# Optimization experiments

Measured on AMD Instinct MI355X. Metric: run time of the kernel, lower is better.

## Reference

```python
import jax, jax.numpy as jnp
import numpy as np

FACTORS = (16, 8, 8)          # prod == n_embd == 1024
H, DK = 16, 64
FACTOR_PARAMS = tuple(f * (f - 1) // 2 for f in FACTORS)  # (120, 28, 28)
DV = sum(FACTOR_PARAMS)       # 176
DVP = 256                     # next power of two padding
B, T, C = 2, 2048, 1024
OFFSET = 64


def _skew_exp(params, f):
    """params: (..., f*(f-1)//2) -> rotation matrices (..., f, f) via expm of skew-sym."""
    rows, cols = np.triu_indices(f, k=1)
    batch = params.shape[:-1]
    mat = jnp.zeros(batch + (f, f), jnp.float32).at[..., rows, cols].set(params.astype(jnp.float32))
    S = mat - jnp.swapaxes(mat, -1, -2)
    R = jax.vmap(jax.scipy.linalg.expm)(S.reshape((-1, f, f)))
    return R.reshape(batch + (f, f))


def setup_inputs() -> dict:
    key = jax.random.key(0)
    k1, k2, k3, k4, k5 = jax.random.split(key, 5)
    return {
        "x": jax.random.normal(k1, (B, T, C), jnp.float32),
        "cached_k": jax.random.normal(k2, (B, H, OFFSET, DK), jnp.float32),
        "cached_v": jax.random.normal(k3, (B, H, OFFSET, DVP), jnp.float32),
        "W_QK": jax.random.normal(k4, (2 * H * DK, C), jnp.float32) * 0.02,
        "W_V": jax.random.normal(k5, (H * DV, C), jnp.float32) * 0.02,
    }


def reference(x, cached_k, cached_v, W_QK, W_V):
    Bx, Tx, Cx = x.shape
    qk = x @ W_QK.T                                  # (B,T,2*H*DK)
    q, k = jnp.split(qk, 2, axis=-1)
    q = q.reshape(Bx, Tx, H, DK).transpose(0, 2, 1, 3)   # (B,H,T,DK)
    k = k.reshape(Bx, Tx, H, DK).transpose(0, 2, 1, 3)
    v = (x @ W_V.T).reshape(Bx, Tx, H, DV).transpose(0, 2, 1, 3)  # (B,H,T,DV)
    v = jnp.pad(v, ((0, 0), (0, 0), (0, 0), (0, DVP - DV)))       # pad to DVP

    offset = cached_k.shape[2]
    k = jnp.concatenate([cached_k, k], axis=2)       # (B,H,offset+T,DK)
    v = jnp.concatenate([cached_v, v], axis=2)       # (B,H,offset+T,DVP)

    neg_inf = jnp.finfo(jnp.float32).min
    causal = jnp.triu(jnp.full((Tx, Tx), neg_inf, jnp.float32), k=1)
    mask = jnp.concatenate([jnp.zeros((Tx, offset), jnp.float32), causal], axis=1)

    scores = jnp.einsum('bhqd,bhkd->bhqk', q, k) * (1.0 / np.sqrt(DK)) + mask
    attn = jax.nn.softmax(scores, axis=-1)
    rot = jnp.einsum('bhqk,bhkd->bhqd', attn, v)[..., :DV]   # (B,H,T,DV)
    rot = rot.transpose(0, 2, 1, 3).sum(axis=2)              # sum over heads -> (B,T,DV)

    splits = jnp.split(rot, np.cumsum(FACTOR_PARAMS)[:-1].tolist(), axis=-1)
    y = x.reshape(Bx, Tx, *FACTORS)
    for i, (p, f) in enumerate(zip(splits, FACTORS)):
        R = _skew_exp(p, f).astype(x.dtype)          # (B,T,f,f)
        y = jnp.moveaxis(y, 2 + i, 2)
        sh = y.shape
        y = (R @ y.reshape(Bx, Tx, f, -1)).reshape(sh)
        y = jnp.moveaxis(y, 2, 2 + i)
    y = y.reshape(Bx, Tx, Cx)
    return y, k, v
```

## Files before the change

kernel.cpp:

```cpp
#include <hip/hip_runtime.h>

typedef _Float16 h8 __attribute__((ext_vector_type(8)));
typedef _Float16 h4 __attribute__((ext_vector_type(4)));
typedef float f4 __attribute__((ext_vector_type(4)));

#define NB 2
#define NT 2048
#define NC 1024
#define NH 16
#define DKK 64
#define DV 176
#define DVP 256
#define OFF 64
#define KV 2112
#define SCALE_Q 0.18033688011112f
#define CLAMP_S 11.541560327111f

__device__ __forceinline__ void load_lds16(const _Float16* g, _Float16* l) {
    __builtin_amdgcn_global_load_lds(
        (const __attribute__((address_space(1))) void*)g,
        (__attribute__((address_space(3))) void*)l, 16, 0, 0);
}

#define PREPA_X   1048576
#define PREPA_QK  1572864
#define PREPA_WV  2293760
#define PREPA_END 2473984
__global__ __launch_bounds__(256)
void k_prep_a(const float* __restrict__ x, const float* __restrict__ wqk,
              const float* __restrict__ wv, _Float16* __restrict__ xh,
              _Float16* __restrict__ wqkh, _Float16* __restrict__ wvh,
              float* __restrict__ rotb) {
    int i = blockIdx.x * 256 + threadIdx.x;
    if (i >= PREPA_END) return;
    if (i < PREPA_X) {
        float4 v = *(const float4*)(x + (size_t)i * 4);
        h4 h = {(_Float16)v.x, (_Float16)v.y, (_Float16)v.z, (_Float16)v.w};
        *(h4*)(xh + (size_t)i * 4) = h;
    } else if (i < PREPA_QK) {
        int j = i - PREPA_X;
        float4 v = *(const float4*)(wqk + (size_t)j * 4);
        h4 h = {(_Float16)v.x, (_Float16)v.y, (_Float16)v.z, (_Float16)v.w};
        *(h4*)(wqkh + (size_t)j * 4) = h;
    } else if (i < PREPA_WV) {
        int j = i - PREPA_QK;
        float4 v = *(const float4*)(wv + (size_t)j * 4);
        h4 h = {(_Float16)v.x, (_Float16)v.y, (_Float16)v.z, (_Float16)v.w};
        *(h4*)(wvh + (size_t)j * 4) = h;
    } else {
        int j = i - PREPA_WV;
        *(float4*)(rotb + (size_t)j * 4) = (float4){0.f, 0.f, 0.f, 0.f};
    }
}

#define PREPB_CK   32768
#define PREPB_CV   163840
#define PREPB_END  1474560
__global__ __launch_bounds__(256)
void k_prep_b(const float* __restrict__ ck, const float* __restrict__ cv,
              float* __restrict__ out_k, _Float16* __restrict__ kh,
              float* __restrict__ out_v, _Float16* __restrict__ vTh) {
    int i = blockIdx.x * 256 + threadIdx.x;
    if (i >= PREPB_END) return;
    if (i < PREPB_CK) {
        int bh = i >> 10, rem = i & 1023;
        int pos = rem >> 4, d4 = (rem & 15) * 4;
        float4 v = *(const float4*)(ck + (size_t)i * 4);
        size_t o = ((size_t)bh * KV + pos) * DKK + d4;
        *(float4*)(out_k + o) = v;
        h4 h = {(_Float16)v.x, (_Float16)v.y, (_Float16)v.z, (_Float16)v.w};
        *(h4*)(kh + o) = h;
    } else if (i < PREPB_CV) {
        int j = i - PREPB_CK;
        int bh = j >> 12, rem = j & 4095;
        int pos = rem >> 6, c4 = (rem & 63) * 4;
        float4 v = *(const float4*)(cv + (size_t)j * 4);
        *(float4*)(out_v + ((size_t)bh * KV + pos) * DVP + c4) = v;
        if (c4 < DV) {
            _Float16* vt = vTh + ((size_t)bh * DV + c4) * KV + pos;
            vt[0]              = (_Float16)v.x;
            vt[KV]             = (_Float16)v.y;
            vt[2 * (size_t)KV] = (_Float16)v.z;
            vt[3 * (size_t)KV] = (_Float16)v.w;
        }
    } else {
        int j = i - PREPB_CV;
        int bh = j / 40960, rem = j - bh * 40960;
        int t = rem / 20, c4 = DV + (rem - t * 20) * 4;
        *(float4*)(out_v + ((size_t)bh * KV + OFF + t) * DVP + c4) = (float4){0.f, 0.f, 0.f, 0.f};
    }
}

__global__ __launch_bounds__(256)
void k_gemm_fused(const _Float16* __restrict__ xh, const _Float16* __restrict__ wh,
                  _Float16* __restrict__ qh, _Float16* __restrict__ kh,
                  float* __restrict__ out_k, _Float16* __restrict__ vTh,
                  float* __restrict__ out_v) {
    __shared__ char smem_raw[36864];
    auto As = (_Float16(*)[64])smem_raw;
    auto Bs = (_Float16(*)[64])(smem_raw + 16384);
    auto Ts = (_Float16(*)[64][72])smem_raw;
    auto Tq = (_Float16(*)[128][68])smem_raw;

    const int tid = threadIdx.x;
    const int lane = tid & 63, w = tid >> 6;
    const int lr = lane & 15, lg = lane >> 4;
    const int wm = w >> 1, wn = w & 1;
    const int n = blockIdx.x, x = n & 7, idx = n >> 3;
    const int mi = (x & 3) * 8 + idx / 19;
    const int ni = (x >> 2) * 19 + idx % 19;
    const int m0 = mi * 128, n0 = ni * 128;
    const int srow = lane >> 3;
    const int sc16 = (lane & 7) ^ srow;

    f4 acc[4][4];
#pragma unroll
    for (int i = 0; i < 4; i++)
#pragma unroll
        for (int j = 0; j < 4; j++) acc[i][j] = (f4){0.f, 0.f, 0.f, 0.f};

    for (int k0 = 0; k0 < NC; k0 += 64) {
        __syncthreads();
#pragma unroll
        for (int j = 0; j < 4; j++) {
            int i = w * 4 + j;
            int row = i * 8 + srow;
            load_lds16(&xh[(size_t)(m0 + row) * NC + k0 + sc16 * 8],
                       (_Float16*)As + i * 512);
            load_lds16(&wh[(size_t)(n0 + row) * NC + k0 + sc16 * 8],
                       (_Float16*)Bs + i * 512);
        }
        asm volatile("s_waitcnt vmcnt(0)" ::: "memory");
        __syncthreads();

#pragma unroll
        for (int ks = 0; ks < 2; ks++) {
            h8 a[4], b[4];
#pragma unroll
            for (int mt = 0; mt < 4; mt++) {
                int row = wm * 64 + mt * 16 + lr;
                a[mt] = *(const h8*)&As[row][((ks * 4 + lg) ^ (lr & 7)) * 8];
            }
#pragma unroll
            for (int nt = 0; nt < 4; nt++) {
                int row = wn * 64 + nt * 16 + lr;
                b[nt] = *(const h8*)&Bs[row][((ks * 4 + lg) ^ (lr & 7)) * 8];
            }
#pragma unroll
            for (int mt = 0; mt < 4; mt++)
#pragma unroll
                for (int nt = 0; nt < 4; nt++)
                    acc[mt][nt] = __builtin_amdgcn_mfma_f32_16x16x32_f16(a[mt], b[nt], acc[mt][nt], 0, 0, 0);
        }
    }

    const int b_ = m0 >> 11;
    const int mloc = m0 & (NT - 1);

    if (ni < 8) {
        __syncthreads();
#pragma unroll
        for (int mt = 0; mt < 4; mt++)
#pragma unroll
            for (int nt = 0; nt < 4; nt++)
#pragma unroll
                for (int r = 0; r < 4; r++)
                    Tq[wn][wm * 64 + mt * 16 + lg * 4 + r][nt * 16 + lr] =
                        (_Float16)(acc[mt][nt][r] * SCALE_Q);
        __syncthreads();
        const int h0 = n0 >> 6;
#pragma unroll
        for (int i = 0; i < 8; i++) {
            int id = i * 256 + tid;
            int hh = id >> 10, rem = id & 1023;
            int t = rem >> 3, dk8 = (rem & 7) * 8;
            h8 v = *(const h8*)&Tq[hh][t][dk8];
            *(h8*)&qh[((size_t)(b_ * NH + h0 + hh) * NT + mloc + t) * DKK + dk8] = v;
        }
    } else if (ni < 16) {
        __syncthreads();
#pragma unroll
        for (int mt = 0; mt < 4; mt++)
#pragma unroll
            for (int nt = 0; nt < 4; nt++)
#pragma unroll
                for (int r = 0; r < 4; r++) {
                    int t = wm * 64 + mt * 16 + lg * 4 + r;
                    int g2 = n0 - 1024 + wn * 64 + nt * 16 + lr;
                    float v = acc[mt][nt][r];
                    int h = g2 >> 6, dk = g2 & 63;
                    out_k[((size_t)(b_ * NH + h) * KV + OFF + mloc + t) * DKK + dk] = v;
                    Tq[wn][t][nt * 16 + lr] = (_Float16)v;
                }
        __syncthreads();
        const int h0 = (n0 - 1024) >> 6;
#pragma unroll
        for (int i = 0; i < 8; i++) {
            int id = i * 256 + tid;
            int hh = id >> 10, rem = id & 1023;
            int t = rem >> 3, dk8 = (rem & 7) * 8;
            h8 v = *(const h8*)&Tq[hh][t][dk8];
            *(h8*)&kh[((size_t)(b_ * NH + h0 + hh) * KV + OFF + mloc + t) * DKK + dk8] = v;
        }
    } else {
        __syncthreads();
#pragma unroll
        for (int mt = 0; mt < 4; mt++)
#pragma unroll
            for (int nt = 0; nt < 4; nt++) {
                h4 ph;
#pragma unroll
                for (int r = 0; r < 4; r++) {
                    int grow = m0 + wm * 64 + mt * 16 + lg * 4 + r;
                    int gcol = n0 - 2048 + wn * 64 + nt * 16 + lr;
                    float v = acc[mt][nt][r];
                    int bb = grow >> 11, t = grow & (NT - 1);
                    int h = gcol / DV;
                    int c = gcol - h * DV;
                    out_v[((size_t)(bb * NH + h) * KV + OFF + t) * DVP + c] = v;
                    ph[r] = (_Float16)v;
                }
                *(h4*)&Ts[w][nt * 16 + lr][mt * 16 + lg * 4] = ph;
            }
        __syncthreads();
        {
            _Float16* vout = vTh + ((size_t)b_ * (NH * DV) + (n0 - 2048)) * KV + OFF + mloc;
            const int seg = tid & 31;
            const int rr = tid >> 5;
#pragma unroll
            for (int i = 0; i < 16; i++) {
                int c = i * 8 + rr;
                int buf = ((seg >> 4) << 1) | (c >> 6);
                h4 vv = *(const h4*)&Ts[buf][c & 63][(seg & 15) * 4];
                *(h4*)&vout[(size_t)c * KV + seg * 4] = vv;
            }
        }
    }
}

__global__ __launch_bounds__(256, 4)
void k_attn(const _Float16* __restrict__ qh, const _Float16* __restrict__ kh,
            const _Float16* __restrict__ vTh, float* __restrict__ rot) {
    __shared__ _Float16 Ks[64][64];
    __shared__ _Float16 Vs[176][64];
    __shared__ _Float16 Ps[4][16][72];
    const int tid = threadIdx.x, lane = tid & 63, w = tid >> 6;
    const int lr = lane & 15, lg = lane >> 4;
    const int n = blockIdx.x;
    const int gq = 31 - (n >> 5);
    const int bh = (n & 7) + 8 * ((n >> 3) & 3);
    const int b_ = bh >> 4;
    const int qt = gq * 4 + w;
    const int q = qt * 16 + lr;

    const _Float16* qp = qh + ((size_t)bh * NT + q) * DKK;
    h8 bq0 = *(const h8*)(qp + lg * 8);
    h8 bq1 = *(const h8*)(qp + 32 + lg * 8);

    const _Float16* kbase = kh + (size_t)bh * KV * DKK;
    const _Float16* vbase = vTh + (size_t)bh * DV * KV;

    f4 o[11];
#pragma unroll
    for (int i = 0; i < 11; i++) o[i] = (f4){0.f, 0.f, 0.f, 0.f};
    float l_acc = 0.f;

    const int nkt = gq + 2;
    const int srow = lane >> 3, sslot = lane & 7;
    const int sc16 = sslot ^ srow;

    for (int kt = 0; kt < nkt; kt++) {
        __syncthreads();
#pragma unroll
        for (int j = 0; j < 2; j++) {
            int i = w * 2 + j;
            int row = i * 8 + srow;
            load_lds16(&kbase[(size_t)(kt * 64 + row) * DKK + sc16 * 8],
                       (_Float16*)Ks + i * 512);
        }
#pragma unroll
        for (int j = 0; j < 6; j++) {
            int i = w * 6 + j;
            if (i < 22) {
                int row = i * 8 + srow;
                load_lds16(&vbase[(size_t)row * KV + kt * 64 + sc16 * 8],
                           (_Float16*)Vs + i * 512);
            }
        }
        asm volatile("s_waitcnt vmcnt(4)" ::: "memory");
        __syncthreads();

        f4 s[4];
#pragma unroll
        for (int nt = 0; nt < 4; nt++) {
            int krow = nt * 16 + lr;
            h8 ak0 = *(const h8*)&Ks[krow][(lg ^ (lr & 7)) * 8];
            h8 ak1 = *(const h8*)&Ks[krow][((4 + lg) ^ (lr & 7)) * 8];
            f4 st = (f4){0.f, 0.f, 0.f, 0.f};
            st = __builtin_amdgcn_mfma_f32_16x16x32_f16(ak0, bq0, st, 0, 0, 0);
            st = __builtin_amdgcn_mfma_f32_16x16x32_f16(ak1, bq1, st, 0, 0, 0);
            s[nt] = st;
        }

#pragma unroll
        for (int nt = 0; nt < 4; nt++) {
            h4 ph;
#pragma unroll
            for (int r = 0; r < 4; r++) {
                int key = kt * 64 + nt * 16 + lg * 4 + r;
                float sv = fminf(s[nt][r], CLAMP_S);
                float p = (key <= q + OFF) ? __builtin_exp2f(sv) : 0.f;
                l_acc += p;
                ph[r] = (_Float16)p;
            }
            *(h4*)&Ps[w][lr][nt * 16 + lg * 4] = ph;
        }

        asm volatile("s_waitcnt vmcnt(0)" ::: "memory");
        __syncthreads();

#pragma unroll
        for (int ks = 0; ks < 2; ks++) {
            h8 ap = *(const h8*)&Ps[w][lr][ks * 32 + lg * 8];
#pragma unroll
            for (int nt = 0; nt < 11; nt++) {
                int vrow = nt * 16 + lr;
                h8 bv = *(const h8*)&Vs[vrow][((ks * 4 + lg) ^ (lr & 7)) * 8];
                o[nt] = __builtin_amdgcn_mfma_f32_16x16x32_f16(ap, bv, o[nt], 0, 0, 0);
            }
        }
    }

    l_acc += __shfl_xor(l_acc, 16);
    l_acc += __shfl_xor(l_acc, 32);
    float lq[4];
#pragma unroll
    for (int r = 0; r < 4; r++) lq[r] = 1.f / __shfl(l_acc, lg * 4 + r);
#pragma unroll
    for (int r = 0; r < 4; r++) {
        int t = qt * 16 + lg * 4 + r;
#pragma unroll
        for (int nt = 0; nt < 11; nt++) {
            atomicAdd(&rot[((size_t)b_ * NT + t) * DV + nt * 16 + lr], o[nt][r] * lq[r]);
        }
    }
}

__device__ __forceinline__ int triu16(int r, int c) { return r * 15 - (r * (r - 1)) / 2 + (c - r - 1); }
__device__ __forceinline__ int triu8(int r, int c)  { return r * 7  - (r * (r - 1)) / 2 + (c - r - 1); }

__global__ __launch_bounds__(64)
void k_rotate(const float* __restrict__ x, const float* __restrict__ rot,
              float* __restrict__ y) {
    __shared__ float A16[16][16], Ta[16][16], Tb[16][16];
    __shared__ float A8[2][8][8], T8a[2][8][8], T8b[2][8][8];
    __shared__ float pbuf[176];
    __shared__ float xt[1024], t1[1024], t2[1024];
    const int tok = blockIdx.x;
    const int lane = threadIdx.x;

    for (int i = lane; i < 176; i += 64) pbuf[i] = rot[(size_t)tok * DV + i];
    for (int i = lane; i < 1024; i += 64) xt[i] = x[(size_t)tok * NC + i];
    __syncthreads();

#pragma unroll
    for (int j = 0; j < 4; j++) {
        int e = lane * 4 + j, r = e >> 4, c = e & 15;
        float v = 0.f;
        if (r < c) v = pbuf[triu16(r, c)];
        else if (r > c) v = -pbuf[triu16(c, r)];
        A16[r][c] = v;
    }
    {
        int r = lane >> 3, c = lane & 7;
#pragma unroll
        for (int m = 0; m < 2; m++) {
            float v = 0.f;
            if (r < c) v = pbuf[120 + m * 28 + triu8(r, c)];
            else if (r > c) v = -pbuf[120 + m * 28 + triu8(c, r)];
            A8[m][r][c] = v;
        }
    }
    __syncthreads();

    float rn = 0.f;
    if (lane < 16) {
#pragma unroll
        for (int c = 0; c < 16; c++) rn += fabsf(A16[lane][c]);
    }
#pragma unroll
    for (int mm = 1; mm < 16; mm <<= 1) rn = fmaxf(rn, __shfl_xor(rn, mm));
    rn = __shfl(rn, 0);
    int s = 0;
    while (rn > 0.5f && s < 60) { rn *= 0.5f; s++; }
    const float sc16 = exp2f((float)(-s));
    __syncthreads();
#pragma unroll
    for (int j = 0; j < 4; j++) { int e = lane * 4 + j; A16[e >> 4][e & 15] *= sc16; }
    __syncthreads();
#pragma unroll
    for (int j = 0; j < 4; j++) {
        int e = lane * 4 + j, r = e >> 4, c = e & 15;
        Ta[r][c] = (r == c ? 1.f : 0.f) + A16[r][c] * (1.f / 12.f);
    }
    __syncthreads();
    float (*Tc)[16] = Ta, (*Tn)[16] = Tb;
    for (int k = 11; k >= 1; k--) {
#pragma unroll
        for (int j = 0; j < 4; j++) {
            int e = lane * 4 + j, r = e >> 4, c = e & 15;
            float acc = 0.f;
#pragma unroll
            for (int q = 0; q < 16; q++) acc += A16[r][q] * Tc[q][c];
            Tn[r][c] = acc * (1.f / (float)k) + (r == c ? 1.f : 0.f);
        }
        __syncthreads();
        float (*tmp)[16] = Tc; Tc = Tn; Tn = tmp;
    }
    for (int it = 0; it < s; it++) {
#pragma unroll
        for (int j = 0; j < 4; j++) {
            int e = lane * 4 + j, r = e >> 4, c = e & 15;
            float acc = 0.f;
#pragma unroll
            for (int q = 0; q < 16; q++) acc += Tc[r][q] * Tc[q][c];
            Tn[r][c] = acc;
        }
        __syncthreads();
        float (*tmp)[16] = Tc; Tc = Tn; Tn = tmp;
    }

    float (*R2p)[8] = T8a[0];
    float (*R3p)[8] = T8a[1];
    {
        int r = lane >> 3, c = lane & 7;
        for (int m = 0; m < 2; m++) {
            float rn8 = 0.f;
            if (lane < 8) {
#pragma unroll
                for (int cc = 0; cc < 8; cc++) rn8 += fabsf(A8[m][lane][cc]);
            }
#pragma unroll
            for (int mm = 1; mm < 8; mm <<= 1) rn8 = fmaxf(rn8, __shfl_xor(rn8, mm));
            rn8 = __shfl(rn8, 0);
            int s8 = 0;
            while (rn8 > 0.5f && s8 < 60) { rn8 *= 0.5f; s8++; }
            float sc8 = exp2f((float)(-s8));
            __syncthreads();
            A8[m][r][c] *= sc8;
            __syncthreads();
            T8a[m][r][c] = (r == c ? 1.f : 0.f) + A8[m][r][c] * (1.f / 12.f);
            __syncthreads();
            float (*tc)[8] = T8a[m], (*tn)[8] = T8b[m];
            for (int k = 11; k >= 1; k--) {
                float acc = 0.f;
#pragma unroll
                for (int q = 0; q < 8; q++) acc += A8[m][r][q] * tc[q][c];
                tn[r][c] = acc * (1.f / (float)k) + (r == c ? 1.f : 0.f);
                __syncthreads();
                float (*tmp)[8] = tc; tc = tn; tn = tmp;
            }
            for (int it = 0; it < s8; it++) {
                float acc = 0.f;
#pragma unroll
                for (int q = 0; q < 8; q++) acc += tc[r][q] * tc[q][c];
                tn[r][c] = acc;
                __syncthreads();
                float (*tmp)[8] = tc; tc = tn; tn = tmp;
            }
            if (m == 0) R2p = tc; else R3p = tc;
        }
    }
    __syncthreads();

    for (int o = lane; o < 1024; o += 64) {
        int c = o & 7, base = o & ~7;
        float acc = 0.f;
#pragma unroll
        for (int j = 0; j < 8; j++) acc += R3p[c][j] * xt[base + j];
        t1[o] = acc;
    }
    __syncthreads();
    for (int o = lane; o < 1024; o += 64) {
        int c = o & 7, bb = (o >> 3) & 7, a = o >> 6;
        float acc = 0.f;
#pragma unroll
        for (int j = 0; j < 8; j++) acc += R2p[bb][j] * t1[a * 64 + j * 8 + c];
        t2[o] = acc;
    }
    __syncthreads();
    for (int o = lane; o < 1024; o += 64) {
        int rr = o & 63, a = o >> 6;
        float acc = 0.f;
#pragma unroll
        for (int j = 0; j < 16; j++) acc += Tc[a][j] * t2[j * 64 + rr];
        y[(size_t)tok * NC + o] = acc;
    }
}

extern "C" void kernel_launch(void* const* d_in, const int* in_sizes, int n_in,
                              void* d_out, int out_size, void* d_ws, size_t ws_size,
                              hipStream_t stream) {
    const float* x   = (const float*)d_in[0];
    const float* ck  = (const float*)d_in[1];
    const float* cv  = (const float*)d_in[2];
    const float* wqk = (const float*)d_in[3];
    const float* wv  = (const float*)d_in[4];

    float* out_y = (float*)d_out;
    float* out_k = out_y + (size_t)NB * NT * NC;
    float* out_v = out_k + (size_t)NB * NH * KV * DKK;

    char* ws = (char*)d_ws;
    _Float16* xh   = (_Float16*)ws;  ws += (size_t)NB * NT * NC * 2;
    _Float16* wqkh = (_Float16*)ws;  ws += (size_t)2 * NH * DKK * NC * 2;
    _Float16* wvh  = (_Float16*)ws;  ws += (size_t)NH * DV * NC * 2;
    _Float16* qh   = (_Float16*)ws;  ws += (size_t)NB * NH * NT * DKK * 2;
    _Float16* kh   = (_Float16*)ws;  ws += (size_t)NB * NH * KV * DKK * 2;
    _Float16* vTh  = (_Float16*)ws;  ws += (size_t)NB * NH * DV * KV * 2;
    float*    rotb = (float*)ws;     ws += (size_t)NB * NT * DV * 4;

    k_prep_a<<<dim3((PREPA_END + 255) / 256), dim3(256), 0, stream>>>(
        x, wqk, wv, xh, wqkh, wvh, rotb);
    k_prep_b<<<dim3((PREPB_END + 255) / 256), dim3(256), 0, stream>>>(
        ck, cv, out_k, kh, out_v, vTh);

    k_gemm_fused<<<dim3(1216), dim3(256), 0, stream>>>(xh, wqkh, qh, kh, out_k, vTh, out_v);

    k_attn<<<dim3(1024), dim3(256), 0, stream>>>(qh, kh, vTh, rotb);

    k_rotate<<<dim3(NB * NT), dim3(64), 0, stream>>>(x, rotb, out_y);
}
```

Measured before the change: 204.2 us.

## Double-buffer GEMM LDS tiles and merge attention tile waits into one barrier

The fused QKV GEMM now uses two LDS buffers (64KB total), so the next K-slice loads into one buffer while MFMAs run on the other. The old per-iteration full load-wait-sync sequence becomes prefetch, partial vmcnt wait and raw barriers. In the attention kernel, the K and V tile loads are both waited on before a single barrier, and the second barrier before the PV MMA is dropped. This is safe because each wave only reads its own P rows. In exchange, the larger LDS footprint lowers how many GEMM blocks fit per CU, and V load latency is no longer hidden behind the score and softmax work.

Result: faster. 191.5 us (-6.2%).

```diff
diff --git a/kernel.cpp b/kernel.cpp
--- a/kernel.cpp
+++ b/kernel.cpp
@@ -96,9 +96,7 @@
                   _Float16* __restrict__ qh, _Float16* __restrict__ kh,
                   float* __restrict__ out_k, _Float16* __restrict__ vTh,
                   float* __restrict__ out_v) {
-    __shared__ char smem_raw[36864];
-    auto As = (_Float16(*)[64])smem_raw;
-    auto Bs = (_Float16(*)[64])(smem_raw + 16384);
+    __shared__ char smem_raw[65536];
     auto Ts = (_Float16(*)[64][72])smem_raw;
     auto Tq = (_Float16(*)[128][68])smem_raw;
 
@@ -119,32 +117,44 @@
 #pragma unroll
         for (int j = 0; j < 4; j++) acc[i][j] = (f4){0.f, 0.f, 0.f, 0.f};
 
-    for (int k0 = 0; k0 < NC; k0 += 64) {
-        __syncthreads();
+    auto stage = [&](int buf, int k0) {
+        _Float16* Ab = (_Float16*)smem_raw + buf * 8192;
+        _Float16* Bb = (_Float16*)(smem_raw + 32768) + buf * 8192;
 #pragma unroll
         for (int j = 0; j < 4; j++) {
             int i = w * 4 + j;
             int row = i * 8 + srow;
-            load_lds16(&xh[(size_t)(m0 + row) * NC + k0 + sc16 * 8],
-                       (_Float16*)As + i * 512);
-            load_lds16(&wh[(size_t)(n0 + row) * NC + k0 + sc16 * 8],
-                       (_Float16*)Bs + i * 512);
-        }
-        asm volatile("s_waitcnt vmcnt(0)" ::: "memory");
-        __syncthreads();
-
+            load_lds16(&xh[(size_t)(m0 + row) * NC + k0 + sc16 * 8], Ab + i * 512);
+            load_lds16(&wh[(size_t)(n0 + row) * NC + k0 + sc16 * 8], Bb + i * 512);
+        }
+    };
+
+    stage(0, 0);
+    int cur = 0;
+    for (int t = 0; t < 16; ++t) {
+        if (t < 15) {
+            stage(cur ^ 1, (t + 1) * 64);
+            asm volatile("s_waitcnt vmcnt(8)" ::: "memory");
+        } else {
+            asm volatile("s_waitcnt vmcnt(0)" ::: "memory");
+        }
+        __builtin_amdgcn_s_barrier();
+        __builtin_amdgcn_sched_barrier(0);
+
+        const _Float16* Ab = (const _Float16*)smem_raw + cur * 8192;
+        const _Float16* Bb = (const _Float16*)(smem_raw + 32768) + cur * 8192;
 #pragma unroll
         for (int ks = 0; ks < 2; ks++) {
             h8 a[4], b[4];
 #pragma unroll
             for (int mt = 0; mt < 4; mt++) {
                 int row = wm * 64 + mt * 16 + lr;
-                a[mt] = *(const h8*)&As[row][((ks * 4 + lg) ^ (lr & 7)) * 8];
+                a[mt] = *(const h8*)&Ab[row * 64 + ((ks * 4 + lg) ^ (lr & 7)) * 8];
             }
 #pragma unroll
             for (int nt = 0; nt < 4; nt++) {
                 int row = wn * 64 + nt * 16 + lr;
-                b[nt] = *(const h8*)&Bs[row][((ks * 4 + lg) ^ (lr & 7)) * 8];
+                b[nt] = *(const h8*)&Bb[row * 64 + ((ks * 4 + lg) ^ (lr & 7)) * 8];
             }
 #pragma unroll
             for (int mt = 0; mt < 4; mt++)
@@ -152,6 +162,9 @@
                 for (int nt = 0; nt < 4; nt++)
                     acc[mt][nt] = __builtin_amdgcn_mfma_f32_16x16x32_f16(a[mt], b[nt], acc[mt][nt], 0, 0, 0);
         }
+        __builtin_amdgcn_sched_barrier(0);
+        __builtin_amdgcn_s_barrier();
+        cur ^= 1;
     }
 
     const int b_ = m0 >> 11;
@@ -287,7 +300,7 @@
                            (_Float16*)Vs + i * 512);
             }
         }
-        asm volatile("s_waitcnt vmcnt(4)" ::: "memory");
+        asm volatile("s_waitcnt vmcnt(0)" ::: "memory");
         __syncthreads();
 
         f4 s[4];
@@ -315,9 +328,6 @@
             }
             *(h4*)&Ps[w][lr][nt * 16 + lg * 4] = ph;
         }
-
-        asm volatile("s_waitcnt vmcnt(0)" ::: "memory");
-        __syncthreads();
 
 #pragma unroll
         for (int ks = 0; ks < 2; ks++) {
```
